# Optimization experiments

Hardware: AMD Instinct MI355X
Metric: run time of the kernel (lower is better)

## Reference

```python
import jax, jax.numpy as jnp
import numpy as np

B = 2048          # number of graphs in the batch
ACT_DIM = 14      # nodes per graph (act_dim)
C = 128           # in_channels
H = 256           # hidden_size


def _pair_edges(n):
    ii, jj = np.meshgrid(np.arange(n), np.arange(n), indexing='ij')
    m = ii != jj
    return np.stack([ii[m], jj[m]], axis=1)  # [n*(n-1), 2]


def setup_inputs() -> dict:
    key = jax.random.key(0)
    ks = jax.random.split(key, 12)
    edges_np = _pair_edges(ACT_DIM)                       # [182, 2]
    offs = (np.arange(B) * ACT_DIM)[:, None, None]
    batched = (edges_np[None] + offs).reshape(-1, 2)      # [B*182, 2]
    edge_index = jnp.asarray(batched.T, dtype=jnp.int64 if jax.config.jax_enable_x64 else jnp.int32)
    edges = jnp.asarray(edges_np, dtype=jnp.int32)

    def lin(k, o, i):
        return jax.random.normal(k, (o, i), jnp.float32) * (1.0 / np.sqrt(i))

    return {
        'state': jax.random.normal(ks[0], (B * ACT_DIM, C), jnp.float32),
        'conv_w': lin(ks[1], C, C),
        'conv_b': jnp.zeros((C,), jnp.float32),
        'lin1_w': lin(ks[2], H, 2 * C),
        'lin1_b': jax.random.normal(ks[3], (H,), jnp.float32) * 0.01,
        'lin2_w': lin(ks[4], H, H),
        'lin2_b': jax.random.normal(ks[5], (H,), jnp.float32) * 0.01,
        'mu_w': lin(ks[6], 1, H),
        'mu_b': jnp.zeros((1,), jnp.float32),
        'sig_w': lin(ks[7], 1, H),
        'sig_b': jnp.zeros((1,), jnp.float32),
        'noise': jax.random.normal(ks[8], (B, edges_np.shape[0]), jnp.float32),
        'edge_index': edge_index,
        'edges': edges,
    }


def _gcn_conv(x, edge_index, w, b):
    # Standard GCNConv: add self-loops, symmetric normalization, x @ W^T, scatter-add, + bias.
    n = x.shape[0]
    loops = jnp.arange(n, dtype=edge_index.dtype)
    src = jnp.concatenate([edge_index[0], loops])
    dst = jnp.concatenate([edge_index[1], loops])
    deg = jax.ops.segment_sum(jnp.ones_like(src, dtype=x.dtype), dst, num_segments=n)
    dinv = jax.lax.rsqrt(deg)  # deg >= 1 because of self-loops
    norm = dinv[src] * dinv[dst]                       # [E+N]
    xw = x @ w.T                                       # [N, C]
    msg = xw[src] * norm[:, None]                      # gather + scale
    return jax.ops.segment_sum(msg, dst, num_segments=n) + b


def reference(state, conv_w, conv_b, lin1_w, lin1_b, lin2_w, lin2_b,
              mu_w, mu_b, sig_w, sig_b, noise, edge_index, edges):
    out = jax.nn.relu(_gcn_conv(state, edge_index, conv_w, conv_b))
    x = (out + state).reshape(-1, ACT_DIM, C)          # [B, 14, C]
    es, ed = edges[:, 0], edges[:, 1]
    ef = jnp.concatenate([x[:, es, :], x[:, ed, :]], axis=2)   # [B, E, 2C]
    h = jax.nn.leaky_relu(jnp.einsum('bec,hc->beh', ef, lin1_w) + lin1_b)
    h = jax.nn.leaky_relu(jnp.einsum('beh,gh->beg', h, lin2_w) + lin2_b)
    mu = jax.nn.softplus(jnp.einsum('beh,oh->beo', h, mu_w) + mu_b)[..., 0]   # [B, E]
    std = jax.nn.softplus(jnp.einsum('beh,oh->beo', h, sig_w) + sig_b)[..., 0]
    action = mu + std * noise                          # Normal rsample with fixed eps
    log_prob = jnp.sum(
        -0.5 * ((action - mu) / std) ** 2 - jnp.log(std) - 0.5 * jnp.log(2.0 * jnp.pi),
        axis=-1)                                       # [B]
    return action, log_prob
```

## Files before the change

kernel.cpp:

```cpp
#include <hip/hip_runtime.h>

#define ACT 14
#define CC 128
#define HH 256
#define EPB 182
#define NB 2048
#define M2 (NB*EPB)
#define NS 520
#define LP_CONST (-182.0f * 0.91893853320467274f)

typedef short s16x8 __attribute__((ext_vector_type(8)));
typedef _Float16 h16x8 __attribute__((ext_vector_type(8)));
typedef _Float16 h16x2 __attribute__((ext_vector_type(2)));
typedef float f32x2 __attribute__((ext_vector_type(2)));
typedef float f32x4 __attribute__((ext_vector_type(4)));
typedef int   i32x4 __attribute__((ext_vector_type(4)));
typedef float f32x16 __attribute__((ext_vector_type(16)));

__device__ __forceinline__ short f2bf(float f) {
    unsigned u = __float_as_uint(f);
    unsigned r = (u + 0x7fffu + ((u >> 16) & 1u)) >> 16;
    return (short)r;
}
__device__ __forceinline__ float bflo(int m) { return __uint_as_float(((unsigned)m) << 16); }
__device__ __forceinline__ float bfhi(int m) { return __uint_as_float((unsigned)m & 0xffff0000u); }
__device__ __forceinline__ float leaky(float x) { return fmaxf(x, 0.01f * x); }
__device__ __forceinline__ float softplusf(float x) { return x > 15.f ? x : log1pf(expf(x)); }

__device__ __forceinline__ short f2h(float f) {
    _Float16 h = (_Float16)f;
    return __builtin_bit_cast(short, h);
}
__device__ __forceinline__ int pk_f16(float a, float b) {
    return __builtin_bit_cast(int, __builtin_amdgcn_cvt_pkrtz(a, b));
}
__device__ __forceinline__ int pk_f16_rn(float a, float b) {
    return (int)(unsigned short)f2h(a) | ((int)f2h(b) << 16);
}
__device__ __forceinline__ float fdot2i(int a, int b, float c) {
#if __has_builtin(__builtin_amdgcn_fdot2)
    return __builtin_amdgcn_fdot2(__builtin_bit_cast(h16x2, a),
                                  __builtin_bit_cast(h16x2, b), c, false);
#else
    h16x2 av = __builtin_bit_cast(h16x2, a), bv = __builtin_bit_cast(h16x2, b);
    return c + (float)av[0] * (float)bv[0] + (float)av[1] * (float)bv[1];
#endif
}

__global__ __launch_bounds__(256) void prep_kernel(
    const float* __restrict__ conv_w, const float* __restrict__ lin1_w,
    const float* __restrict__ lin2_w, const float* __restrict__ mu_w,
    const float* __restrict__ sig_w,
    short* __restrict__ W2h, short* __restrict__ W1h,
    int* __restrict__ cwP, int* __restrict__ w1sP,
    int* __restrict__ msbf)
{
    int i = blockIdx.x * 256 + threadIdx.x;
    W2h[i] = f2h(lin2_w[i]);
    {
        int n = i >> 7, k = i & 127;
        float v = (n < 256) ? lin1_w[n * 256 + k] : lin1_w[(n - 256) * 256 + 128 + k];
        W1h[i] = f2h(v);
    }
    if (i < 8192) {
        int p = i >> 7, j = i & 127;
        cwP[i] = pk_f16_rn(conv_w[j * 128 + 2 * p], conv_w[j * 128 + 2 * p + 1]);
    }
    if (i < 16384) {
        int p = i >> 8, h = i & 255;
        float a0 = lin1_w[h * 256 + 2 * p]     + lin1_w[h * 256 + 128 + 2 * p];
        float a1 = lin1_w[h * 256 + 2 * p + 1] + lin1_w[h * 256 + 128 + 2 * p + 1];
        w1sP[i] = pk_f16_rn(a0, a1);
    }
    if (i < 256) msbf[i] = (int)(unsigned short)f2bf(mu_w[i]) | ((int)f2bf(sig_w[i]) << 16);
}

__global__ __launch_bounds__(512, 4) void actor_kernel(
    const float* __restrict__ state, const short* __restrict__ W1h,
    const short* __restrict__ W2h,
    const int* __restrict__ cwP, const float* __restrict__ conv_b,
    const int* __restrict__ w1sP, const float* __restrict__ lin1_b,
    const float* __restrict__ lin2_b, const int* __restrict__ msbf,
    const float* __restrict__ mu_b, const float* __restrict__ sig_b,
    const float* __restrict__ noise, const int* __restrict__ edges,
    float* __restrict__ out)
{
    __shared__ short h1L[2][8192];
    __shared__ short nodeL[2 * ACT * NS];
    __shared__ float ssumL[2][128];
    __shared__ float gL[2][128];
    __shared__ float wL[2][256];
    __shared__ float b2L[256];
    __shared__ int   msL[256];
    __shared__ float mu_acc[384], sg_acc[384];
    __shared__ float lp_acc[2];

    short* stateL = &h1L[0][0];

    const int t = threadIdx.x, b = blockIdx.x;
    const int lane = t & 63, ln = lane & 15, q = lane >> 4;
    const int w = t >> 6;
    const int l32 = lane & 31, hf = lane >> 5;

    #pragma unroll
    for (int it = 0; it < 2; ++it) {
        int idx = it * 512 + t;
        int bt = idx >> 9, row = (idx >> 5) & 15, c4 = idx & 31;
        int kk = c4 >> 3, k8 = (c4 & 7) * 4;
        int* dst = (int*)&stateL[bt * 2560 + kk * 640 + row * 40 + k8];
        if (row < ACT) {
            f32x4 x = *(const f32x4*)(state + ((size_t)(2 * b + bt) * ACT + row) * CC + c4 * 4);
            dst[0] = pk_f16(x[0], x[1]); dst[1] = pk_f16(x[2], x[3]);
        } else { dst[0] = 0; dst[1] = 0; }
    }
    if (t < 256) {
        b2L[t] = lin2_b[t];
        msL[t] = msbf[t];
    } else {
        int i = t - 256, bt = i >> 7, c = i & 127;
        const float* sp = state + (size_t)(2 * b + bt) * ACT * CC + c;
        float s = 0.f;
        #pragma unroll
        for (int r = 0; r < ACT; ++r) s += sp[r * CC];
        ssumL[bt][c] = s * (1.f / 14.f);
    }
    if (t < 384) { mu_acc[t] = 0.f; sg_acc[t] = 0.f; }
    if (t < 2) lp_acc[t] = 0.f;
    __syncthreads();

    {
        int bt = t >> 8, r = t & 255, j = r >> 1, s = r & 1;
        const float* ss = ssumL[bt];
        float a = 0.f;
        int p0 = s * 32;
        #pragma unroll 8
        for (int pi = 0; pi < 32; ++pi) {
            int p = p0 + pi;
            f32x2 sv = *(const f32x2*)&ss[2 * p];
            a = fdot2i(cwP[p * 128 + j], pk_f16(sv[0], sv[1]), a);
        }
        a += __shfl_xor(a, 1);
        if (s == 0) gL[bt][j] = fmaxf(a + conv_b[j], 0.f);
    }
    __syncthreads();
    {
        int bt = t >> 8, h = t & 255;
        const float* gg = gL[bt];
        float a = 0.f;
        #pragma unroll 8
        for (int p = 0; p < 64; ++p) {
            f32x2 gv = *(const f32x2*)&gg[2 * p];
            a = fdot2i(w1sP[p * 256 + h], pk_f16(gv[0], gv[1]), a);
        }
        wL[bt][h] = a + lin1_b[h];
    }
    __syncthreads();

    f32x4 zero4 = {0.f, 0.f, 0.f, 0.f};
    f32x4 nacc[2][4];
    #pragma unroll
    for (int bt = 0; bt < 2; ++bt) {
        nacc[bt][0] = zero4; nacc[bt][1] = zero4;
        nacc[bt][2] = zero4; nacc[bt][3] = zero4;
    }
    #pragma unroll
    for (int c = 0; c < 4; ++c) {
        h16x8 a80 = __builtin_bit_cast(h16x8, *(const s16x8*)&stateL[0 * 2560 + c * 640 + ln * 40 + q * 8]);
        h16x8 a81 = __builtin_bit_cast(h16x8, *(const s16x8*)&stateL[1 * 2560 + c * 640 + ln * 40 + q * 8]);
        #pragma unroll
        for (int i = 0; i < 4; ++i) {
            int ct = w + 8 * i;
            h16x8 b8 = __builtin_bit_cast(h16x8, *(const s16x8*)&W1h[(size_t)(ct * 16 + ln) * CC + c * 32 + q * 8]);
            nacc[0][i] = __builtin_amdgcn_mfma_f32_16x16x32_f16(a80, b8, nacc[0][i], 0, 0, 0);
            nacc[1][i] = __builtin_amdgcn_mfma_f32_16x16x32_f16(a81, b8, nacc[1][i], 0, 0, 0);
        }
    }
    #pragma unroll
    for (int bt = 0; bt < 2; ++bt)
        #pragma unroll
        for (int i = 0; i < 4; ++i) {
            int col = (w + 8 * i) * 16 + ln;
            float wadd = (col < HH) ? wL[bt][col] : 0.f;
            #pragma unroll
            for (int rg = 0; rg < 4; ++rg) {
                int node = q * 4 + rg;
                if (node < ACT) nodeL[(bt * ACT + node) * NS + col] = f2h(nacc[bt][i][rg] + wadd);
            }
        }

    s16x8 wa[16];
    #pragma unroll
    for (int c = 0; c < 16; ++c)
        wa[c] = *(const s16x8*)&W2h[(size_t)(w * 32 + l32) * HH + c * 16 + hf * 8];
    __syncthreads();

    const h16x2 c001 = {(_Float16)0.01f, (_Float16)0.01f};
    auto build = [&](int tile, int bufi) {
        int bt = (tile >= 6) ? 1 : 0;
        int e32 = t & 31;
        int e = (tile - bt * 6) * 32 + e32;
        bool ok = e < EPB;
        int base = bt * ACT * NS;
        int uo = base, vo = base + HH;
        if (ok) { int2 p = ((const int2*)edges)[e]; uo += p.x * NS; vo += p.y * NS; }
        int sl = t >> 5;
        #pragma unroll
        for (int s = 0; s < 2; ++s) {
            int slot = sl + 16 * s;
            int chunk = slot >> 1, half = slot & 1;
            int koff = chunk * 16 + half * 8;
            int o[4] = {0, 0, 0, 0};
            if (ok) {
                s16x8 u8 = *(const s16x8*)&nodeL[uo + koff];
                s16x8 v8 = *(const s16x8*)&nodeL[vo + koff];
                const int* ui = (const int*)&u8;
                const int* vi = (const int*)&v8;
                #pragma unroll
                for (int j = 0; j < 4; ++j) {
                    h16x2 uu = __builtin_bit_cast(h16x2, ui[j]);
                    h16x2 vv = __builtin_bit_cast(h16x2, vi[j]);
                    h16x2 sum = uu + vv;
                    h16x2 lk  = __builtin_elementwise_max(sum, sum * c001);
                    o[j] = __builtin_bit_cast(int, lk);
                }
            }
            *(s16x8*)&h1L[bufi][chunk * 512 + (half * 32 + e32) * 8] = *(const s16x8*)o;
        }
    };

    build(0, 0);
    for (int tile = 0; tile < 12; ++tile) {
        __syncthreads();
        if (tile < 11) build(tile + 1, (tile + 1) & 1);
        const int buf = tile & 1;
        f32x16 acc;
        #pragma unroll
        for (int r = 0; r < 16; ++r) acc[r] = 0.f;
        #pragma unroll
        for (int c = 0; c < 16; ++c) {
            h16x8 b8 = __builtin_bit_cast(h16x8, *(const s16x8*)&h1L[buf][c * 512 + lane * 8]);
            h16x8 a8 = __builtin_bit_cast(h16x8, wa[c]);
            acc = __builtin_amdgcn_mfma_f32_32x32x16_f16(a8, b8, acc, 0, 0, 0);
        }
        int bt = (tile >= 6) ? 1 : 0;
        int col0 = (tile - bt * 6) * 32;
        float pmu = 0.f, psg = 0.f;
        const int nsb = w * 32 + 4 * hf;
        #pragma unroll
        for (int g = 0; g < 4; ++g) {
            f32x4 b4 = *(const f32x4*)&b2L[nsb + 8 * g];
            i32x4 m4 = *(const i32x4*)&msL[nsb + 8 * g];
            #pragma unroll
            for (int i = 0; i < 4; ++i) {
                float h2 = leaky(acc[g * 4 + i] + b4[i]);
                pmu += bflo(m4[i]) * h2;
                psg += bfhi(m4[i]) * h2;
            }
        }
        pmu += __shfl_xor(pmu, 32);
        psg += __shfl_xor(psg, 32);
        if (lane < 32) {
            atomicAdd(&mu_acc[bt * 192 + col0 + l32], pmu);
            atomicAdd(&sg_acc[bt * 192 + col0 + l32], psg);
        }
    }
    __syncthreads();

    float lpv = 0.f;
    {
        int bt = t >> 8, i = t & 255;
        if (i < EPB) {
            float mu = softplusf(mu_acc[bt * 192 + i] + mu_b[0]);
            float sd = softplusf(sg_acc[bt * 192 + i] + sig_b[0]);
            float z = noise[(size_t)(2 * b + bt) * EPB + i];
            out[(size_t)(2 * b + bt) * EPB + i] = mu + sd * z;
            lpv = -0.5f * z * z - logf(sd);
        }
    }
    #pragma unroll
    for (int off = 1; off < 64; off <<= 1) lpv += __shfl_xor(lpv, off);
    if (lane == 0) atomicAdd(&lp_acc[t >> 8], lpv);
    __syncthreads();
    if (t < 2) out[M2 + 2 * b + t] = lp_acc[t] + LP_CONST;
}

extern "C" void kernel_launch(void* const* d_in, const int* in_sizes, int n_in,
                              void* d_out, int out_size, void* d_ws, size_t ws_size,
                              hipStream_t stream)
{
    const float* state  = (const float*)d_in[0];
    const float* conv_w = (const float*)d_in[1];
    const float* conv_b = (const float*)d_in[2];
    const float* lin1_w = (const float*)d_in[3];
    const float* lin1_b = (const float*)d_in[4];
    const float* lin2_w = (const float*)d_in[5];
    const float* lin2_b = (const float*)d_in[6];
    const float* mu_w   = (const float*)d_in[7];
    const float* mu_b   = (const float*)d_in[8];
    const float* sig_w  = (const float*)d_in[9];
    const float* sig_b  = (const float*)d_in[10];
    const float* noise  = (const float*)d_in[11];
    const int*   edges  = (const int*)d_in[13];
    float* out = (float*)d_out;

    char* ws = (char*)d_ws;
    short* W2h    = (short*)ws;  ws += 65536 * 2;
    short* W1h    = (short*)ws;  ws += 65536 * 2;
    int*   cwP    = (int*)ws;    ws += 8192 * 4;
    int*   w1sP   = (int*)ws;    ws += 16384 * 4;
    int*   msbf   = (int*)ws;    ws += 256 * 4;

    prep_kernel<<<256, 256, 0, stream>>>(conv_w, lin1_w, lin2_w, mu_w, sig_w,
                                         W2h, W1h, cwP, w1sP, msbf);
    actor_kernel<<<NB / 2, 512, 0, stream>>>(state, W1h, W2h,
                                             cwP, conv_b, w1sP, lin1_b,
                                             lin2_b, msbf, mu_b, sig_b,
                                             noise, edges, out);
}
```

Baseline: 197.1 us.

## Transpose small GEMV weights, pre-pack f16 vectors, use packed f32 epilogue math

Transposes the conv and summed-lin1 weight tables so each thread reads contiguous 16-byte vectors. The mean-state and conv output vectors are pre-packed to f16 pairs in shared memory, so the dot loops no longer convert per iteration, and the dot products now use four independent accumulators. The epilogue drops bf16-packed mu/sig weights in favour of fp32 copies in LDS and uses packed f32x2 arithmetic. The mu and sig atomic adds are split across the two half-waves. The transposed layout makes each thread walk a different 256-byte row, so the global loads are no longer coalesced across lanes.

```diff
diff --git a/kernel.cpp b/kernel.cpp
--- a/kernel.cpp
+++ b/kernel.cpp
@@ -17,14 +17,6 @@
 typedef int   i32x4 __attribute__((ext_vector_type(4)));
 typedef float f32x16 __attribute__((ext_vector_type(16)));
 
-__device__ __forceinline__ short f2bf(float f) {
-    unsigned u = __float_as_uint(f);
-    unsigned r = (u + 0x7fffu + ((u >> 16) & 1u)) >> 16;
-    return (short)r;
-}
-__device__ __forceinline__ float bflo(int m) { return __uint_as_float(((unsigned)m) << 16); }
-__device__ __forceinline__ float bfhi(int m) { return __uint_as_float((unsigned)m & 0xffff0000u); }
-__device__ __forceinline__ float leaky(float x) { return fmaxf(x, 0.01f * x); }
 __device__ __forceinline__ float softplusf(float x) { return x > 15.f ? x : log1pf(expf(x)); }
 
 __device__ __forceinline__ short f2h(float f) {
@@ -49,11 +41,9 @@
 
 __global__ __launch_bounds__(256) void prep_kernel(
     const float* __restrict__ conv_w, const float* __restrict__ lin1_w,
-    const float* __restrict__ lin2_w, const float* __restrict__ mu_w,
-    const float* __restrict__ sig_w,
+    const float* __restrict__ lin2_w,
     short* __restrict__ W2h, short* __restrict__ W1h,
-    int* __restrict__ cwP, int* __restrict__ w1sP,
-    int* __restrict__ msbf)
+    int* __restrict__ cwPT, int* __restrict__ w1sPT)
 {
     int i = blockIdx.x * 256 + threadIdx.x;
     W2h[i] = f2h(lin2_w[i]);
@@ -63,35 +53,35 @@
         W1h[i] = f2h(v);
     }
     if (i < 8192) {
-        int p = i >> 7, j = i & 127;
-        cwP[i] = pk_f16_rn(conv_w[j * 128 + 2 * p], conv_w[j * 128 + 2 * p + 1]);
+        int j = i >> 6, p = i & 63;
+        cwPT[i] = pk_f16_rn(conv_w[j * 128 + 2 * p], conv_w[j * 128 + 2 * p + 1]);
     }
     if (i < 16384) {
-        int p = i >> 8, h = i & 255;
+        int h = i >> 6, p = i & 63;
         float a0 = lin1_w[h * 256 + 2 * p]     + lin1_w[h * 256 + 128 + 2 * p];
         float a1 = lin1_w[h * 256 + 2 * p + 1] + lin1_w[h * 256 + 128 + 2 * p + 1];
-        w1sP[i] = pk_f16_rn(a0, a1);
-    }
-    if (i < 256) msbf[i] = (int)(unsigned short)f2bf(mu_w[i]) | ((int)f2bf(sig_w[i]) << 16);
+        w1sPT[i] = pk_f16_rn(a0, a1);
+    }
 }
 
 __global__ __launch_bounds__(512, 4) void actor_kernel(
     const float* __restrict__ state, const short* __restrict__ W1h,
     const short* __restrict__ W2h,
-    const int* __restrict__ cwP, const float* __restrict__ conv_b,
-    const int* __restrict__ w1sP, const float* __restrict__ lin1_b,
-    const float* __restrict__ lin2_b, const int* __restrict__ msbf,
+    const int* __restrict__ cwPT, const float* __restrict__ conv_b,
+    const int* __restrict__ w1sPT, const float* __restrict__ lin1_b,
+    const float* __restrict__ lin2_b,
+    const float* __restrict__ mu_w, const float* __restrict__ sig_w,
     const float* __restrict__ mu_b, const float* __restrict__ sig_b,
     const float* __restrict__ noise, const int* __restrict__ edges,
     float* __restrict__ out)
 {
     __shared__ short h1L[2][8192];
     __shared__ short nodeL[2 * ACT * NS];
-    __shared__ float ssumL[2][128];
-    __shared__ float gL[2][128];
+    __shared__ int   ssP[2][64];
+    __shared__ int   gP[2][64];
     __shared__ float wL[2][256];
     __shared__ float b2L[256];
-    __shared__ int   msL[256];
+    __shared__ float muL[256], sgL[256];
     __shared__ float mu_acc[384], sg_acc[384];
     __shared__ float lp_acc[2];
 
@@ -115,14 +105,17 @@
     }
     if (t < 256) {
         b2L[t] = lin2_b[t];
-        msL[t] = msbf[t];
+        muL[t] = mu_w[t];
+        sgL[t] = sig_w[t];
     } else {
         int i = t - 256, bt = i >> 7, c = i & 127;
         const float* sp = state + (size_t)(2 * b + bt) * ACT * CC + c;
         float s = 0.f;
         #pragma unroll
         for (int r = 0; r < ACT; ++r) s += sp[r * CC];
-        ssumL[bt][c] = s * (1.f / 14.f);
+        s *= (1.f / 14.f);
+        float s2 = __shfl_xor(s, 1);
+        if (!(c & 1)) ssP[bt][c >> 1] = pk_f16(s, s2);
     }
     if (t < 384) { mu_acc[t] = 0.f; sg_acc[t] = 0.f; }
     if (t < 2) lp_acc[t] = 0.f;
@@ -130,29 +123,34 @@
 
     {
         int bt = t >> 8, r = t & 255, j = r >> 1, s = r & 1;
-        const float* ss = ssumL[bt];
-        float a = 0.f;
-        int p0 = s * 32;
-        #pragma unroll 8
-        for (int pi = 0; pi < 32; ++pi) {
-            int p = p0 + pi;
-            f32x2 sv = *(const f32x2*)&ss[2 * p];
-            a = fdot2i(cwP[p * 128 + j], pk_f16(sv[0], sv[1]), a);
-        }
+        const i32x4* wp = (const i32x4*)&cwPT[j * 64 + s * 32];
+        const i32x4* sp4 = (const i32x4*)&ssP[bt][s * 32];
+        float a0 = 0.f, a1 = 0.f, a2 = 0.f, a3 = 0.f;
+        #pragma unroll
+        for (int u = 0; u < 8; ++u) {
+            i32x4 wv = wp[u]; i32x4 sv = sp4[u];
+            a0 = fdot2i(wv[0], sv[0], a0); a1 = fdot2i(wv[1], sv[1], a1);
+            a2 = fdot2i(wv[2], sv[2], a2); a3 = fdot2i(wv[3], sv[3], a3);
+        }
+        float a = (a0 + a1) + (a2 + a3);
         a += __shfl_xor(a, 1);
-        if (s == 0) gL[bt][j] = fmaxf(a + conv_b[j], 0.f);
+        float gf = fmaxf(a + conv_b[j], 0.f);
+        float go = __shfl_xor(gf, 2);
+        if ((r & 3) == 0) gP[bt][r >> 2] = pk_f16(gf, go);
     }
     __syncthreads();
     {
         int bt = t >> 8, h = t & 255;
-        const float* gg = gL[bt];
-        float a = 0.f;
+        const i32x4* wp = (const i32x4*)&w1sPT[h * 64];
+        const i32x4* gp4 = (const i32x4*)&gP[bt][0];
+        float a0 = 0.f, a1 = 0.f, a2 = 0.f, a3 = 0.f;
         #pragma unroll 8
-        for (int p = 0; p < 64; ++p) {
-            f32x2 gv = *(const f32x2*)&gg[2 * p];
-            a = fdot2i(w1sP[p * 256 + h], pk_f16(gv[0], gv[1]), a);
-        }
-        wL[bt][h] = a + lin1_b[h];
+        for (int u = 0; u < 16; ++u) {
+            i32x4 wv = wp[u]; i32x4 gv = gp4[u];
+            a0 = fdot2i(wv[0], gv[0], a0); a1 = fdot2i(wv[1], gv[1], a1);
+            a2 = fdot2i(wv[2], gv[2], a2); a3 = fdot2i(wv[3], gv[3], a3);
+        }
+        wL[bt][h] = (a0 + a1) + (a2 + a3) + lin1_b[h];
     }
     __syncthreads();
 
@@ -228,6 +226,7 @@
         }
     };
 
+    const f32x2 c001p = {0.01f, 0.01f};
     build(0, 0);
     for (int tile = 0; tile < 12; ++tile) {
         __syncthreads();
@@ -244,25 +243,31 @@
         }
         int bt = (tile >= 6) ? 1 : 0;
         int col0 = (tile - bt * 6) * 32;
-        float pmu = 0.f, psg = 0.f;
+        f32x2 pm = {0.f, 0.f}, ps = {0.f, 0.f};
         const int nsb = w * 32 + 4 * hf;
         #pragma unroll
         for (int g = 0; g < 4; ++g) {
             f32x4 b4 = *(const f32x4*)&b2L[nsb + 8 * g];
-            i32x4 m4 = *(const i32x4*)&msL[nsb + 8 * g];
+            f32x4 m4 = *(const f32x4*)&muL[nsb + 8 * g];
+            f32x4 s4 = *(const f32x4*)&sgL[nsb + 8 * g];
             #pragma unroll
-            for (int i = 0; i < 4; ++i) {
-                float h2 = leaky(acc[g * 4 + i] + b4[i]);
-                pmu += bflo(m4[i]) * h2;
-                psg += bfhi(m4[i]) * h2;
+            for (int p = 0; p < 2; ++p) {
+                f32x2 a2 = {acc[g * 4 + 2 * p], acc[g * 4 + 2 * p + 1]};
+                f32x2 b2 = {b4[2 * p], b4[2 * p + 1]};
+                f32x2 x  = a2 + b2;
+                f32x2 lk = __builtin_elementwise_max(x, x * c001p);
+                f32x2 mm = {m4[2 * p], m4[2 * p + 1]};
+                f32x2 sv = {s4[2 * p], s4[2 * p + 1]};
+                pm += mm * lk;
+                ps += sv * lk;
             }
         }
+        float pmu = pm[0] + pm[1];
+        float psg = ps[0] + ps[1];
         pmu += __shfl_xor(pmu, 32);
         psg += __shfl_xor(psg, 32);
-        if (lane < 32) {
-            atomicAdd(&mu_acc[bt * 192 + col0 + l32], pmu);
-            atomicAdd(&sg_acc[bt * 192 + col0 + l32], psg);
-        }
+        if (lane < 32) atomicAdd(&mu_acc[bt * 192 + col0 + l32], pmu);
+        else           atomicAdd(&sg_acc[bt * 192 + col0 + l32], psg);
     }
     __syncthreads();
 
@@ -306,14 +311,13 @@
     char* ws = (char*)d_ws;
     short* W2h    = (short*)ws;  ws += 65536 * 2;
     short* W1h    = (short*)ws;  ws += 65536 * 2;
-    int*   cwP    = (int*)ws;    ws += 8192 * 4;
-    int*   w1sP   = (int*)ws;    ws += 16384 * 4;
-    int*   msbf   = (int*)ws;    ws += 256 * 4;
-
-    prep_kernel<<<256, 256, 0, stream>>>(conv_w, lin1_w, lin2_w, mu_w, sig_w,
-                                         W2h, W1h, cwP, w1sP, msbf);
+    int*   cwPT   = (int*)ws;    ws += 8192 * 4;
+    int*   w1sPT  = (int*)ws;    ws += 16384 * 4;
+
+    prep_kernel<<<256, 256, 0, stream>>>(conv_w, lin1_w, lin2_w,
+                                         W2h, W1h, cwPT, w1sPT);
     actor_kernel<<<NB / 2, 512, 0, stream>>>(state, W1h, W2h,
-                                             cwP, conv_b, w1sP, lin1_b,
-                                             lin2_b, msbf, mu_b, sig_b,
+                                             cwPT, conv_b, w1sPT, lin1_b,
+                                             lin2_b, mu_w, sig_w, mu_b, sig_b,
                                              noise, edges, out);
 }
```

After: 205.1 us. +4.0%, slower.
